# Optimization experiments

Hardware: AMD Instinct MI355X
Metric: run time of the kernel (lower is better)

Reference implementation:

```python
import jax, jax.numpy as jnp
import numpy as np
import math

B, S, D_MODEL, H = 4, 256, 2048, 256
HEAD_DIM = D_MODEL // H  # 8


def setup_inputs() -> dict:
    key = jax.random.key(0)
    ks = jax.random.split(key, 10)
    w_scale = 0.02
    inp = {
        "x": jax.random.normal(ks[0], (B, S, D_MODEL), dtype=jnp.float32),
        "phase_shift": jax.random.normal(ks[1], (H, 1, 1), dtype=jnp.float32),
        "Wq": jax.random.normal(ks[2], (D_MODEL, D_MODEL), dtype=jnp.float32) * w_scale,
        "bq": jnp.zeros((D_MODEL,), dtype=jnp.float32),
        "Wk": jax.random.normal(ks[3], (D_MODEL, D_MODEL), dtype=jnp.float32) * w_scale,
        "bk": jnp.zeros((D_MODEL,), dtype=jnp.float32),
        "Wv": jax.random.normal(ks[4], (D_MODEL, D_MODEL), dtype=jnp.float32) * w_scale,
        "bv": jnp.zeros((D_MODEL,), dtype=jnp.float32),
        "Wo": jax.random.normal(ks[5], (D_MODEL, D_MODEL), dtype=jnp.float32) * w_scale,
        "bo": jnp.zeros((D_MODEL,), dtype=jnp.float32),
    }
    return inp


def _forward(x, phase_shift, Wq, bq, Wk, bk, Wv, bv, Wo, bo):
    b, s, dm = x.shape
    h = phase_shift.shape[0]
    d = dm // h
    # projections (torch Linear with random weights; stored as [in,out])
    q = (x @ Wq + bq).reshape(b, s, h, d)
    k = (x @ Wk + bk).reshape(b, s, h, d)
    v = (x @ Wv + bv).reshape(b, s, h, d)
    # complex phase rotation: q *= exp(+i phi), k *= exp(-i phi)
    # phase_shift (h,1,1) broadcasts against (b,s,h,d) -> varies along the s dim (requires s==h)
    c = jnp.cos(phase_shift)  # (h,1,1)
    sn = jnp.sin(phase_shift)
    qr, qi = q * c, q * sn          # Re/Im of rotated q
    kr, ki = k * c, -(k * sn)       # Re/Im of rotated k
    scale = 1.0 / math.sqrt(d)
    # per-(b,s) head-mixing scores: [b,s,h,h], complex matmul split into real/imag
    sr = (jnp.einsum('bshd,bsgd->bshg', qr, kr)
          - jnp.einsum('bshd,bsgd->bshg', qi, ki)) * scale
    si = (jnp.einsum('bshd,bsgd->bshg', qr, ki)
          + jnp.einsum('bshd,bsgd->bshg', qi, kr)) * scale  # analytically 0 (phases cancel)
    attn_r = jax.nn.softmax(sr, axis=-1)
    attn_i = jax.nn.softmax(si, axis=-1)  # faithful dual softmax; v is real so only
    # Re(attention @ v) = attn_r @ v reaches the output (.real is taken before o_proj)
    del attn_i
    out = jnp.einsum('bshg,bsgd->bshd', attn_r, v).reshape(b, s, dm)
    return out @ Wo + bo


def reference(x, phase_shift, Wq, bq, Wk, bk, Wv, bv, Wo, bo):
    return _forward(x, phase_shift, Wq, bq, Wk, bk, Wv, bv, Wo, bo)
```

## Files before the change

### kernel.cpp

```cpp
#include <hip/hip_runtime.h>
#include <math.h>

#define M_TOK 1024
#define DM    2048
#define NH    256
#define HD    8
#define SCALE 0.35355339059327373f

typedef _Float16 f16x8 __attribute__((ext_vector_type(8)));
typedef _Float16 f16x4 __attribute__((ext_vector_type(4)));
typedef float    f32x4 __attribute__((ext_vector_type(4)));

__global__ __launch_bounds__(256) void prep(
    const float* __restrict__ x, _Float16* __restrict__ xh,
    const float* __restrict__ W0, const float* __restrict__ W1,
    const float* __restrict__ W2, const float* __restrict__ W3,
    _Float16* __restrict__ T0, _Float16* __restrict__ T1,
    _Float16* __restrict__ T2, _Float16* __restrict__ T3)
{
    __shared__ float t[64][65];
    const int tid = threadIdx.x;
    const int z   = blockIdx.z;

    if (z == 4) {
        const int i = (blockIdx.y * 32 + blockIdx.x) * 256 + tid;
        const float4 a = ((const float4*)x)[2 * i];
        const float4 b = ((const float4*)x)[2 * i + 1];
        f16x8 v;
        v[0] = (_Float16)a.x; v[1] = (_Float16)a.y; v[2] = (_Float16)a.z; v[3] = (_Float16)a.w;
        v[4] = (_Float16)b.x; v[5] = (_Float16)b.y; v[6] = (_Float16)b.z; v[7] = (_Float16)b.w;
        ((f16x8*)xh)[i] = v;
        return;
    }

    const float* W = (z == 0) ? W0 : (z == 1) ? W1 : (z == 2) ? W2 : W3;
    _Float16*    T = (z == 0) ? T0 : (z == 1) ? T1 : (z == 2) ? T2 : T3;

    const int nb = blockIdx.x * 64;
    const int kb = blockIdx.y * 64;
    const int tr = tid >> 4;
    const int tc = (tid & 15) << 2;

    #pragma unroll
    for (int rr = 0; rr < 4; ++rr) {
        const int k = kb + rr * 16 + tr;
        const float4 v = *(const float4*)&W[(size_t)k * DM + nb + tc];
        t[rr * 16 + tr][tc + 0] = v.x;
        t[rr * 16 + tr][tc + 1] = v.y;
        t[rr * 16 + tr][tc + 2] = v.z;
        t[rr * 16 + tr][tc + 3] = v.w;
    }
    __syncthreads();
    #pragma unroll
    for (int rr = 0; rr < 4; ++rr) {
        const int n = nb + rr * 16 + tr;
        f16x4 v;
        #pragma unroll
        for (int j = 0; j < 4; ++j)
            v[j] = (_Float16)t[tc + j][rr * 16 + tr];
        *(f16x4*)&T[(size_t)n * DM + kb + tc] = v;
    }
}

template<int WGR, int WGC, int WTR, int WTC, bool F16OUT>
__global__ __launch_bounds__(256, 3) void gemm_db(
    const _Float16* __restrict__ A,
    const _Float16* __restrict__ Bt0, const float* __restrict__ b0, void* __restrict__ C0,
    const _Float16* __restrict__ Bt1, const float* __restrict__ b1, void* __restrict__ C1,
    const _Float16* __restrict__ Bt2, const float* __restrict__ b2, void* __restrict__ C2)
{
    constexpr int BM  = WGR * WTR * 16;
    constexpr int BN  = WGC * WTC * 16;
    static_assert(BN == 128, "col tile must be 128");
    constexpr int NA  = BM / 8;
    constexpr int NB  = 16;
    constexpr int NC  = NA + NB;
    constexpr int CPW = NC / 4;
    static_assert(NC % 4 == 0);
    constexpr int BUF = (BM + 128) * 64;

    __shared__ _Float16 smem[2 * BUF];

    const int which = blockIdx.x >> 4;
    const int bn    = (blockIdx.x & 15) * 128;
    const int bm    = blockIdx.y * BM;

    const _Float16* Bt   = (which == 0) ? Bt0 : (which == 1) ? Bt1 : Bt2;
    const float*    bias = (which == 0) ? b0  : (which == 1) ? b1  : b2;
    void*           C    = (which == 0) ? C0  : (which == 1) ? C1  : C2;

    const int tid  = threadIdx.x;
    const int lane = tid & 63;
    const int wv   = tid >> 6;
    const int wr   = (wv / WGC) * (WTR * 16);
    const int wc   = (wv % WGC) * (WTC * 16);
    const int lr   = lane & 15;
    const int lk   = lane >> 4;
    const int rx   = lr & 7;

    const _Float16* gsrc[CPW];
    int             loff[CPW];
    #pragma unroll
    for (int p = 0; p < CPW; ++p) {
        const int c   = wv * CPW + p;
        const int kch = ((lane & 7) ^ (lane >> 3)) << 3;
        if (c < NA) {
            const int rl = c * 8 + (lane >> 3);
            gsrc[p] = A + (size_t)(bm + rl) * DM + kch;
            loff[p] = c * 512 + lane * 8;
        } else {
            const int rl = (c - NA) * 8 + (lane >> 3);
            gsrc[p] = Bt + (size_t)(bn + rl) * DM + kch;
            loff[p] = BM * 64 + (c - NA) * 512 + lane * 8;
        }
    }

    int offA[WTR][2], offB[WTC][2];
    #pragma unroll
    for (int ks = 0; ks < 2; ++ks) {
        const int sw = (((ks << 2) | lk) ^ rx) << 3;
        #pragma unroll
        for (int i = 0; i < WTR; ++i)
            offA[i][ks] = (wr + i * 16 + lr) * 64 + sw;
        #pragma unroll
        for (int j = 0; j < WTC; ++j)
            offB[j][ks] = BM * 64 + (wc + j * 16 + lr) * 64 + sw;
    }

    f32x4 acc[WTR][WTC] = {};

    auto prefetch = [&](int buf) {
        #pragma unroll
        for (int p = 0; p < CPW; ++p) {
            __builtin_amdgcn_global_load_lds(
                (const __attribute__((address_space(1))) void*)gsrc[p],
                (__attribute__((address_space(3))) void*)(smem + buf * BUF + loff[p]),
                16, 0, 0);
            gsrc[p] += 64;
        }
    };

    auto compute = [&](int buf) {
        const _Float16* base = smem + buf * BUF;
        #pragma unroll
        for (int ks = 0; ks < 2; ++ks) {
            f16x8 aF[WTR], bF[WTC];
            #pragma unroll
            for (int i = 0; i < WTR; ++i)
                aF[i] = *(const f16x8*)&base[offA[i][ks]];
            #pragma unroll
            for (int j = 0; j < WTC; ++j)
                bF[j] = *(const f16x8*)&base[offB[j][ks]];
            #pragma unroll
            for (int i = 0; i < WTR; ++i)
                #pragma unroll
                for (int j = 0; j < WTC; ++j)
                    acc[i][j] = __builtin_amdgcn_mfma_f32_16x16x32_f16(aF[i], bF[j], acc[i][j], 0, 0, 0);
        }
    };

    prefetch(0);
    #pragma unroll 1
    for (int it2 = 0; it2 < 16; ++it2) {
        __syncthreads();
        prefetch(1);
        compute(0);
        __syncthreads();
        if (it2 < 15) prefetch(0);
        compute(1);
    }

    #pragma unroll
    for (int i = 0; i < WTR; ++i) {
        #pragma unroll
        for (int j = 0; j < WTC; ++j) {
            const int col = bn + wc + j * 16 + lr;
            const float bv = bias[col];
            #pragma unroll
            for (int r = 0; r < 4; ++r) {
                const int row = bm + wr + i * 16 + lk * 4 + r;
                const float v = acc[i][j][r] + bv;
                if (F16OUT)
                    ((_Float16*)C)[(size_t)row * DM + col] = (_Float16)v;
                else
                    ((float*)C)[(size_t)row * DM + col] = v;
            }
        }
    }
}

__global__ __launch_bounds__(256) void attn_mfma(
    const _Float16* __restrict__ Qh, const _Float16* __restrict__ Kh,
    const _Float16* __restrict__ Vh, _Float16* __restrict__ Oh)
{
    __shared__ _Float16 Vt[8][264];
    __shared__ _Float16 Al[256][72];
    __shared__ _Float16 Ot[256][8];

    const int t    = blockIdx.x;
    const int tid  = threadIdx.x;
    const int lane = tid & 63;
    const int wv   = tid >> 6;
    const int col  = lane & 15;
    const int quad = lane >> 4;
    const int hbase = wv * 64;

    const _Float16* qb = Qh + (size_t)t * DM;
    const _Float16* kb = Kh + (size_t)t * DM;
    const _Float16* vb = Vh + (size_t)t * DM;

    {
        const f16x8 v = *(const f16x8*)(vb + tid * 8);
        #pragma unroll
        for (int d = 0; d < 8; ++d) Vt[d][tid] = v[d];
    }

    f16x8 qf[4];
    #pragma unroll
    for (int ht = 0; ht < 4; ++ht) {
        f16x8 v = {};
        if (quad == 0)
            v = *(const f16x8*)(qb + (hbase + ht * 16 + col) * 8);
        #pragma unroll
        for (int j = 0; j < 8; ++j) qf[ht][j] = v[j] * (_Float16)SCALE;
    }

    __syncthreads();

    const f32x4 zf = {};
    float rsum[4] = {};
    f32x4 oacc[4] = {};

    #pragma unroll 1
    for (int c = 0; c < 4; ++c) {
        const int gchunk = c * 64;

        f16x8 kf[4];
        #pragma unroll
        for (int gt = 0; gt < 4; ++gt) {
            f16x8 v = {};
            if (quad == 0)
                v = *(const f16x8*)(kb + (gchunk + gt * 16 + col) * 8);
            kf[gt] = v;
        }

        f32x4 s[4][4];
        #pragma unroll
        for (int gt = 0; gt < 4; ++gt)
            #pragma unroll
            for (int ht = 0; ht < 4; ++ht)
                s[gt][ht] = __builtin_amdgcn_mfma_f32_16x16x32_f16(kf[gt], qf[ht], zf, 0, 0, 0);

        #pragma unroll
        for (int gt = 0; gt < 4; ++gt) {
            #pragma unroll
            for (int ht = 0; ht < 4; ++ht) {
                f16x4 e4;
                #pragma unroll
                for (int r = 0; r < 4; ++r) {
                    e4[r] = (_Float16)__expf(s[gt][ht][r]);
                    rsum[ht] += (float)e4[r];
                }
                *(f16x4*)&Al[hbase + ht * 16 + col][gt * 16 + quad * 4] = e4;
            }
        }

        #pragma unroll
        for (int ks = 0; ks < 2; ++ks) {
            f16x8 vf = {};
            if (col < 8)
                vf = *(const f16x8*)&Vt[col][gchunk + ks * 32 + quad * 8];
            #pragma unroll
            for (int ht = 0; ht < 4; ++ht) {
                const f16x8 af = *(const f16x8*)&Al[hbase + ht * 16 + col][ks * 32 + quad * 8];
                oacc[ht] = __builtin_amdgcn_mfma_f32_16x16x32_f16(af, vf, oacc[ht], 0, 0, 0);
            }
        }
    }

    #pragma unroll
    for (int ht = 0; ht < 4; ++ht) {
        rsum[ht] += __shfl_xor(rsum[ht], 16, 64);
        rsum[ht] += __shfl_xor(rsum[ht], 32, 64);
    }

    #pragma unroll
    for (int ht = 0; ht < 4; ++ht) {
        #pragma unroll
        for (int r = 0; r < 4; ++r) {
            const float sh = __shfl(rsum[ht], quad * 4 + r, 64);
            const float v  = oacc[ht][r] / sh;
            if (col < 8)
                Ot[hbase + ht * 16 + quad * 4 + r][col] = (_Float16)v;
        }
    }
    const f16x8 ov = *(const f16x8*)&Ot[tid][0];
    *(f16x8*)(Oh + (size_t)t * DM + tid * 8) = ov;
}

extern "C" void kernel_launch(void* const* d_in, const int* in_sizes, int n_in,
                              void* d_out, int out_size, void* d_ws, size_t ws_size,
                              hipStream_t stream)
{
    const float* x  = (const float*)d_in[0];
    const float* Wq = (const float*)d_in[2];
    const float* bq = (const float*)d_in[3];
    const float* Wk = (const float*)d_in[4];
    const float* bk = (const float*)d_in[5];
    const float* Wv = (const float*)d_in[6];
    const float* bv = (const float*)d_in[7];
    const float* Wo = (const float*)d_in[8];
    const float* bo = (const float*)d_in[9];
    float* out = (float*)d_out;

    char* ws = (char*)d_ws;
    _Float16* xh  = (_Float16*)(ws);
    _Float16* Wtq = (_Float16*)(ws + (4u  << 20));
    _Float16* Wtk = (_Float16*)(ws + (12u << 20));
    _Float16* Wtv = (_Float16*)(ws + (20u << 20));
    _Float16* Wto = (_Float16*)(ws + (28u << 20));
    _Float16* Qh  = (_Float16*)(ws + (36u << 20));
    _Float16* Kh  = (_Float16*)(ws + (40u << 20));
    _Float16* Vh  = (_Float16*)(ws + (44u << 20));
    _Float16* Oh  = (_Float16*)(ws + (48u << 20));

    prep<<<dim3(32, 32, 5), dim3(256), 0, stream>>>(
        x, xh, Wq, Wk, Wv, Wo, Wtq, Wtk, Wtv, Wto);

    gemm_db<2, 2, 2, 4, true><<<dim3(48, 16), dim3(256), 0, stream>>>(xh,
        Wtq, bq, (void*)Qh,
        Wtk, bk, (void*)Kh,
        Wtv, bv, (void*)Vh);

    attn_mfma<<<dim3(M_TOK), dim3(256), 0, stream>>>(Qh, Kh, Vh, Oh);

    gemm_db<1, 4, 2, 2, false><<<dim3(16, 32), dim3(256), 0, stream>>>(Oh,
        Wto, bo, (void*)out,
        Wto, bo, (void*)out,
        Wto, bo, (void*)out);
}
```

Measured before the change: 195.4 us.

## Fuse QKV weights into one wide GEMM with larger tiles and use exp2 softmax

The three projection weight matrices now sit contiguously, so the QKV projection runs as a single 1024x6144 GEMM with a 128x96 tile (a 64x8 grid) writing an interleaved QKV buffer. Occupancy drops to 2 waves per SIMD, and the bias is chosen per column range. The attention kernel reads Q, K and V from the interleaved rows, and the softmax folds log2e into the Q scale so it can use a hardware exp2. The larger tiles mean more reuse per block but fewer blocks and more register pressure.

New measurement: 196.8 us. No clear change (+0.7%).

```diff
diff --git a/kernel.cpp b/kernel.cpp
--- a/kernel.cpp
+++ b/kernel.cpp
@@ -6,10 +6,20 @@
 #define NH    256
 #define HD    8
 #define SCALE 0.35355339059327373f
+#define LOG2E 1.4426950408889634f
 
 typedef _Float16 f16x8 __attribute__((ext_vector_type(8)));
 typedef _Float16 f16x4 __attribute__((ext_vector_type(4)));
 typedef float    f32x4 __attribute__((ext_vector_type(4)));
+
+#if defined(__has_builtin)
+#  if __has_builtin(__builtin_amdgcn_exp2f)
+#    define EXP2(x) __builtin_amdgcn_exp2f(x)
+#  endif
+#endif
+#ifndef EXP2
+#  define EXP2(x) exp2f(x)
+#endif
 
 __global__ __launch_bounds__(256) void prep(
     const float* __restrict__ x, _Float16* __restrict__ xh,
@@ -62,32 +72,26 @@
     }
 }
 
-template<int WGR, int WGC, int WTR, int WTC, bool F16OUT>
-__global__ __launch_bounds__(256, 3) void gemm_db(
+template<int WGR, int WGC, int WTR, int WTC, bool F16OUT, int MINW, int CS>
+__global__ __launch_bounds__(256, MINW) void gemm_db(
     const _Float16* __restrict__ A,
-    const _Float16* __restrict__ Bt0, const float* __restrict__ b0, void* __restrict__ C0,
-    const _Float16* __restrict__ Bt1, const float* __restrict__ b1, void* __restrict__ C1,
-    const _Float16* __restrict__ Bt2, const float* __restrict__ b2, void* __restrict__ C2)
+    const _Float16* __restrict__ Bt,
+    const float* __restrict__ b0, const float* __restrict__ b1,
+    const float* __restrict__ b2, void* __restrict__ C)
 {
     constexpr int BM  = WGR * WTR * 16;
     constexpr int BN  = WGC * WTC * 16;
-    static_assert(BN == 128, "col tile must be 128");
     constexpr int NA  = BM / 8;
-    constexpr int NB  = 16;
+    constexpr int NB  = BN / 8;
     constexpr int NC  = NA + NB;
     constexpr int CPW = NC / 4;
     static_assert(NC % 4 == 0);
-    constexpr int BUF = (BM + 128) * 64;
+    constexpr int BUF = (BM + BN) * 64;
 
     __shared__ _Float16 smem[2 * BUF];
 
-    const int which = blockIdx.x >> 4;
-    const int bn    = (blockIdx.x & 15) * 128;
-    const int bm    = blockIdx.y * BM;
-
-    const _Float16* Bt   = (which == 0) ? Bt0 : (which == 1) ? Bt1 : Bt2;
-    const float*    bias = (which == 0) ? b0  : (which == 1) ? b1  : b2;
-    void*           C    = (which == 0) ? C0  : (which == 1) ? C1  : C2;
+    const int bn = blockIdx.x * BN;
+    const int bm = blockIdx.y * BM;
 
     const int tid  = threadIdx.x;
     const int lane = tid & 63;
@@ -175,23 +179,28 @@
         #pragma unroll
         for (int j = 0; j < WTC; ++j) {
             const int col = bn + wc + j * 16 + lr;
-            const float bv = bias[col];
+            float bv;
+            if constexpr (CS > DM) {
+                const float* bp = (col < 2048) ? b0 : (col < 4096) ? b1 : b2;
+                bv = bp[col & 2047];
+            } else {
+                bv = b0[col];
+            }
             #pragma unroll
             for (int r = 0; r < 4; ++r) {
                 const int row = bm + wr + i * 16 + lk * 4 + r;
                 const float v = acc[i][j][r] + bv;
                 if (F16OUT)
-                    ((_Float16*)C)[(size_t)row * DM + col] = (_Float16)v;
+                    ((_Float16*)C)[(size_t)row * CS + col] = (_Float16)v;
                 else
-                    ((float*)C)[(size_t)row * DM + col] = v;
+                    ((float*)C)[(size_t)row * CS + col] = v;
             }
         }
     }
 }
 
 __global__ __launch_bounds__(256) void attn_mfma(
-    const _Float16* __restrict__ Qh, const _Float16* __restrict__ Kh,
-    const _Float16* __restrict__ Vh, _Float16* __restrict__ Oh)
+    const _Float16* __restrict__ QKV, _Float16* __restrict__ Oh)
 {
     __shared__ _Float16 Vt[8][264];
     __shared__ _Float16 Al[256][72];
@@ -205,9 +214,9 @@
     const int quad = lane >> 4;
     const int hbase = wv * 64;
 
-    const _Float16* qb = Qh + (size_t)t * DM;
-    const _Float16* kb = Kh + (size_t)t * DM;
-    const _Float16* vb = Vh + (size_t)t * DM;
+    const _Float16* qb = QKV + (size_t)t * (3 * DM);
+    const _Float16* kb = qb + DM;
+    const _Float16* vb = qb + 2 * DM;
 
     {
         const f16x8 v = *(const f16x8*)(vb + tid * 8);
@@ -222,7 +231,7 @@
         if (quad == 0)
             v = *(const f16x8*)(qb + (hbase + ht * 16 + col) * 8);
         #pragma unroll
-        for (int j = 0; j < 8; ++j) qf[ht][j] = v[j] * (_Float16)SCALE;
+        for (int j = 0; j < 8; ++j) qf[ht][j] = v[j] * (_Float16)(SCALE * LOG2E);
     }
 
     __syncthreads();
@@ -258,7 +267,7 @@
                 f16x4 e4;
                 #pragma unroll
                 for (int r = 0; r < 4; ++r) {
-                    e4[r] = (_Float16)__expf(s[gt][ht][r]);
+                    e4[r] = (_Float16)EXP2(s[gt][ht][r]);
                     rsum[ht] += (float)e4[r];
                 }
                 *(f16x4*)&Al[hbase + ht * 16 + col][gt * 16 + quad * 4] = e4;
@@ -315,27 +324,20 @@
 
     char* ws = (char*)d_ws;
     _Float16* xh  = (_Float16*)(ws);
-    _Float16* Wtq = (_Float16*)(ws + (4u  << 20));
-    _Float16* Wtk = (_Float16*)(ws + (12u << 20));
-    _Float16* Wtv = (_Float16*)(ws + (20u << 20));
+    _Float16* Wt  = (_Float16*)(ws + (4u  << 20));
     _Float16* Wto = (_Float16*)(ws + (28u << 20));
-    _Float16* Qh  = (_Float16*)(ws + (36u << 20));
-    _Float16* Kh  = (_Float16*)(ws + (40u << 20));
-    _Float16* Vh  = (_Float16*)(ws + (44u << 20));
+    _Float16* QKV = (_Float16*)(ws + (36u << 20));
     _Float16* Oh  = (_Float16*)(ws + (48u << 20));
 
     prep<<<dim3(32, 32, 5), dim3(256), 0, stream>>>(
-        x, xh, Wq, Wk, Wv, Wo, Wtq, Wtk, Wtv, Wto);
-
-    gemm_db<2, 2, 2, 4, true><<<dim3(48, 16), dim3(256), 0, stream>>>(xh,
-        Wtq, bq, (void*)Qh,
-        Wtk, bk, (void*)Kh,
-        Wtv, bv, (void*)Vh);
-
-    attn_mfma<<<dim3(M_TOK), dim3(256), 0, stream>>>(Qh, Kh, Vh, Oh);
-
-    gemm_db<1, 4, 2, 2, false><<<dim3(16, 32), dim3(256), 0, stream>>>(Oh,
-        Wto, bo, (void*)out,
-        Wto, bo, (void*)out,
-        Wto, bo, (void*)out);
+        x, xh, Wq, Wk, Wv, Wo,
+        Wt, Wt + 2048 * 2048, Wt + 2 * 2048 * 2048, Wto);
+
+    gemm_db<2, 2, 4, 3, true, 2, 3 * DM><<<dim3(64, 8), dim3(256), 0, stream>>>(
+        xh, Wt, bq, bk, bv, (void*)QKV);
+
+    attn_mfma<<<dim3(M_TOK), dim3(256), 0, stream>>>(QKV, Oh);
+
+    gemm_db<1, 4, 2, 2, false, 3, DM><<<dim3(16, 32), dim3(256), 0, stream>>>(
+        Oh, Wto, bo, bo, bo, (void*)out);
 }
```
